# Performance work log

Measured on AMD Instinct MI355X. Metric: run time of the kernel, lower is better.

## Reference

```python
import math
import jax, jax.numpy as jnp
import numpy as np

NUM_BUCKETS = 32
MAX_DISTANCE = 128
N_HEADS = 16
D_KV = 64


def _relative_position_bucket(relative_position, num_buckets=NUM_BUCKETS, max_distance=MAX_DISTANCE):
    # bidirectional (encoder) version, faithful to T5Attention._relative_position_bucket
    nb = num_buckets // 2
    rel_buckets = (relative_position > 0).astype(jnp.int32) * nb
    rp = jnp.abs(relative_position)
    max_exact = nb // 2
    is_small = rp < max_exact
    # log-spaced buckets for large distances; clamp arg of log to >=1 to avoid -inf
    rp_large = max_exact + (
        jnp.log(jnp.maximum(rp, 1).astype(jnp.float32) / max_exact)
        / math.log(max_distance / max_exact)
        * (nb - max_exact)
    ).astype(jnp.int32)
    rp_large = jnp.minimum(rp_large, nb - 1)
    return rel_buckets + jnp.where(is_small, rp, rp_large)


def setup_inputs() -> dict:
    key = jax.random.key(0)
    ks = jax.random.split(key, 6)
    B, S, D = 2, 2048, 1024
    scale = 0.02
    return {
        "hidden_states": jax.random.normal(ks[0], (B, S, D), dtype=jnp.float32),
        "Wq": jax.random.normal(ks[1], (D, N_HEADS * D_KV), dtype=jnp.float32) * scale,
        "Wk": jax.random.normal(ks[2], (D, N_HEADS * D_KV), dtype=jnp.float32) * scale,
        "Wv": jax.random.normal(ks[3], (D, N_HEADS * D_KV), dtype=jnp.float32) * scale,
        "Wo": jax.random.normal(ks[4], (N_HEADS * D_KV, D), dtype=jnp.float32) * scale,
        "rel_bias": jax.random.normal(ks[5], (NUM_BUCKETS, N_HEADS), dtype=jnp.float32),
    }


def reference(hidden_states, Wq, Wk, Wv, Wo, rel_bias):
    B, S, D = hidden_states.shape
    H, dk = N_HEADS, D_KV
    q = (hidden_states @ Wq).reshape(B, S, H, dk)
    k = (hidden_states @ Wk).reshape(B, S, H, dk)
    v = (hidden_states @ Wv).reshape(B, S, H, dk)

    pos = jnp.arange(S)
    relative_position = pos[None, :] - pos[:, None]          # [S_q, S_k]
    buckets = _relative_position_bucket(relative_position)    # [S_q, S_k]
    bias = rel_bias[buckets].transpose(2, 0, 1)               # [H, S_q, S_k]

    # T5 attention: NO 1/sqrt(d) scaling
    scores = jnp.einsum('bqhd,bkhd->bhqk', q, k) + bias[None]
    attn = jax.nn.softmax(scores, axis=-1)
    ctx = jnp.einsum('bhqk,bkhd->bqhd', attn, v).reshape(B, S, H * dk)
    return ctx @ Wo
```

## Files before the change

kernel.cpp:

```cpp
#include <hip/hip_runtime.h>
#include <hip/hip_bf16.h>
#include <stdint.h>

#define S_LEN 2048
#define NH 16
#define NB_DELTA (2*S_LEN-1)
#define LOG2E 1.4426950408889634f

typedef __attribute__((ext_vector_type(8))) __bf16 bf16x8;
typedef __attribute__((ext_vector_type(4))) float f32x4;

__device__ __forceinline__ unsigned short f2bf(float f){
    union { float f; unsigned int u; } v; v.f = f;
    unsigned int u = v.u;
    return (unsigned short)((u + 0x7FFFu + ((u >> 16) & 1u)) >> 16);
}
__device__ __forceinline__ float bf2f(unsigned short u){
    union { unsigned int u; float f; } v; v.u = ((unsigned int)u) << 16;
    return v.f;
}
__device__ __forceinline__ unsigned int pkbf(float a, float b){
    __hip_bfloat162 h = __float22bfloat162_rn(float2{a, b});
    unsigned int u;
    __builtin_memcpy(&u, &h, 4);
    return u;
}
#if __has_builtin(__builtin_amdgcn_exp2f)
__device__ __forceinline__ float fexp2(float x){ return __builtin_amdgcn_exp2f(x); }
#else
__device__ __forceinline__ float fexp2(float x){ return __expf(x * 0.69314718056f); }
#endif

__device__ __forceinline__ void gload16(const void* g, void* l){
    __builtin_amdgcn_global_load_lds(
        (const __attribute__((address_space(1))) void*)(uintptr_t)g,
        (__attribute__((address_space(3))) void*)(uintptr_t)l, 16, 0, 0);
}

__global__ __launch_bounds__(256) void prep_kernel(
    const float* __restrict__ hs, unsigned short* __restrict__ hsb,
    const float* __restrict__ W0, const float* __restrict__ W1,
    const float* __restrict__ W2, const float* __restrict__ W3,
    unsigned short* __restrict__ D0, unsigned short* __restrict__ D1,
    unsigned short* __restrict__ D2, unsigned short* __restrict__ D3,
    const float* __restrict__ rel_bias, float* __restrict__ biasT){
    if (blockIdx.z == 4) {
        int bi = blockIdx.y * 32 + blockIdx.x;
        for (int it = 0; it < 4; it++) {
            int i = bi * 4096 + it * 1024 + threadIdx.x * 4;
            float4 f = *(const float4*)(hs + i);
            ushort4 o;
            o.x = f2bf(f.x); o.y = f2bf(f.y); o.z = f2bf(f.z); o.w = f2bf(f.w);
            *(ushort4*)(hsb + i) = o;
        }
        if (bi < 16) {
            int t = bi * 256 + threadIdx.x;
            if (t < NB_DELTA) {
                int delta = t - (S_LEN - 1);
                int bucket = (delta > 0) ? 16 : 0;
                int a = delta < 0 ? -delta : delta;
                int b;
                if (a < 8) b = a;
                else {
                    int bl = 33 - __builtin_clz(a * a);
                    b = bl < 15 ? bl : 15;
                }
                bucket += b;
                for (int h = 0; h < NH; h++)
                    biasT[h * NB_DELTA + t] = (rel_bias[bucket * NH + h] - 16.f) * LOG2E;
            }
        }
        return;
    }
    const float* src; unsigned short* dst;
    switch (blockIdx.z) {
        case 0: src = W0; dst = D0; break;
        case 1: src = W1; dst = D1; break;
        case 2: src = W2; dst = D2; break;
        default: src = W3; dst = D3; break;
    }
    __shared__ float tile[32][33];
    int bx = blockIdx.x, by = blockIdx.y;
    int tx = threadIdx.x & 31, ty = threadIdx.x >> 5;
    for (int i = 0; i < 4; i++)
        tile[ty + 8*i][tx] = src[(size_t)(by*32 + ty + 8*i) * 1024 + bx*32 + tx];
    __syncthreads();
    for (int i = 0; i < 4; i++)
        dst[(size_t)(bx*32 + ty + 8*i) * 1024 + by*32 + tx] = f2bf(tile[tx][ty + 8*i]);
}

template<int MODE, int BM>
__global__ __launch_bounds__(256) void gemm_bt_kernel(const unsigned short* __restrict__ A,
                                                      const unsigned short* __restrict__ BT,
                                                      float* __restrict__ C0,
                                                      unsigned short* __restrict__ C1,
                                                      unsigned short* __restrict__ Vt,
                                                      int Kdim, int ldc){
    constexpr int IT = BM / 32;
    __shared__ __align__(16) unsigned short As[BM * 64];
    __shared__ __align__(16) unsigned short Bs[128 * 64];
    const int t = threadIdx.x;
    const int wave = t >> 6, lane = t & 63;
    const int quad = lane >> 4, l16 = lane & 15;
    const int wm = (wave >> 1) * (BM / 2), wn = (wave & 1) * 64;
    const size_t row0 = (size_t)blockIdx.y * BM, col0 = (size_t)blockIdx.x * 128;

    const int srow8 = lane >> 3;
    const int gg = (lane & 7) ^ srow8;
    const unsigned short* gA = A  + (row0 + wave * 8 + srow8) * (size_t)Kdim + gg * 8;
    const unsigned short* gB = BT + (col0 + wave * 8 + srow8) * (size_t)Kdim + gg * 8;

    f32x4 acc[IT][4] = {};

    for (int kt = 0; kt < Kdim; kt += 64) {
        for (int p = 0; p < BM / 32; p++)
            gload16(gA + (size_t)(p * 32) * Kdim + kt, &As[(p * 32 + wave * 8) * 64]);
        for (int p = 0; p < 4; p++)
            gload16(gB + (size_t)(p * 32) * Kdim + kt, &Bs[(p * 32 + wave * 8) * 64]);
        __syncthreads();
        bf16x8 a[2][IT], b[2][4];
        for (int ks = 0; ks < 2; ks++) {
            for (int i = 0; i < IT; i++)
                a[ks][i] = *(const bf16x8*)(&As[(wm + i*16 + l16) * 64 + (((ks*4 + quad) ^ (l16 & 7)) * 8)]);
            for (int j = 0; j < 4; j++)
                b[ks][j] = *(const bf16x8*)(&Bs[(wn + j*16 + l16) * 64 + (((ks*4 + quad) ^ (l16 & 7)) * 8)]);
        }
        for (int ks = 0; ks < 2; ks++)
            for (int i = 0; i < IT; i++)
                for (int j = 0; j < 4; j++)
                    acc[i][j] = __builtin_amdgcn_mfma_f32_16x16x32_bf16(a[ks][i], b[ks][j], acc[i][j], 0, 0, 0);
        __syncthreads();
    }
    for (int i = 0; i < IT; i++)
        for (int j = 0; j < 4; j++) {
            size_t r0 = row0 + wm + i*16 + quad*4;
            size_t c  = col0 + wn + j*16 + l16;
            if (MODE == 0) {
                for (int r = 0; r < 4; r++)
                    C0[(r0 + r) * ldc + c] = acc[i][j][r];
            } else if (c < 2048) {
                float qs = (c < 1024) ? LOG2E : 1.0f;
                for (int r = 0; r < 4; r++)
                    C1[(r0 + r) * ldc + c] = f2bf(acc[i][j][r] * qs);
            } else {
                size_t bb = r0 >> 11, s = r0 & 2047;
                ushort4 o;
                o.x = f2bf(acc[i][j][0]); o.y = f2bf(acc[i][j][1]);
                o.z = f2bf(acc[i][j][2]); o.w = f2bf(acc[i][j][3]);
                *(ushort4*)(Vt + ((bb << 10) + (c - 2048)) * 2048 + s) = o;
            }
        }
}

__global__ __launch_bounds__(512, 4) void flash13_kernel(
    const unsigned short* __restrict__ qkv,
    const unsigned short* __restrict__ vt,
    const float* __restrict__ biasT,
    unsigned short* __restrict__ ctxpb,
    float* __restrict__ rsbuf)
{
    const int qt = blockIdx.x, h = blockIdx.y;
    const int b = blockIdx.z >> 1, ck = blockIdx.z & 1;
    const int kt0 = ck << 10;
    const int t = threadIdx.x;
    const int w = t >> 6, lane = t & 63, quad = lane >> 4, l16 = lane & 15;
    const int q0 = qt * 256;

    __shared__ __align__(16) unsigned short Ks[2][64 * 64];
    __shared__ __align__(16) unsigned short Vs[2][64 * 64];
    __shared__ float bias_b[1280];

    {
        const float* bsrc = biasT + h * NB_DELTA + (kt0 - q0 + 1792);
        for (int u = t; u < 1279; u += 512) bias_b[u] = bsrc[u];
    }
    const int srow8 = lane >> 3;
    const int gg = (lane & 7) ^ srow8;
    const int swz = (l16 & 7) * 8;
    const unsigned short* kbase = qkv + (size_t)(b * S_LEN + w * 8 + srow8) * 3072 + 1024 + h * 64 + gg * 8;
    const unsigned short* vbase = vt + (size_t)(b * 1024 + h * 64 + w * 8 + srow8) * 2048 + gg * 8;
    gload16(kbase + (size_t)kt0 * 3072, &Ks[0][(w * 8) * 64]);
    gload16(vbase + kt0,                &Vs[0][(w * 8) * 64]);

    bf16x8 qb[2][2];
    {
        const unsigned short* qbase =
            qkv + (size_t)(b * S_LEN + q0 + w * 32 + l16) * 3072 + h * 64 + quad * 8;
        for (int nt = 0; nt < 2; nt++)
            for (int ks = 0; ks < 2; ks++)
                qb[ks][nt] = *(const bf16x8*)(qbase + (size_t)nt * 16 * 3072 + ks * 32);
    }
    __syncthreads();

    bf16x8 onesA = {};
    if (l16 == 0) {
        const __bf16 one = (__bf16)1.0f;
        for (int e = 0; e < 8; e++) onesA[e] = one;
    }

    f32x4 ctx[4][2] = {};
    f32x4 rsacc[2] = {};
    const int ib0 = 255 + quad * 4 - w * 32 - l16;

    int cur = 0;
    for (int i = 0; i < 16; i++) {
        if (i < 15) {
            int ktn = kt0 + (i + 1) * 64;
            gload16(kbase + (size_t)ktn * 3072, &Ks[cur ^ 1][(w * 8) * 64]);
            gload16(vbase + ktn,                &Vs[cur ^ 1][(w * 8) * 64]);
        }
        f32x4 st[4][2];
        const int ibt = ib0 + i * 64;
        for (int nt = 0; nt < 2; nt++)
            for (int nb = 0; nb < 4; nb++) {
                const float* bp = &bias_b[ibt - nt * 16 + nb * 16];
                st[nb][nt][0] = bp[0]; st[nb][nt][1] = bp[1];
                st[nb][nt][2] = bp[2]; st[nb][nt][3] = bp[3];
            }
        __builtin_amdgcn_s_setprio(1);
        for (int ks = 0; ks < 2; ks++)
            for (int nb = 0; nb < 4; nb++) {
                bf16x8 ka = *(const bf16x8*)&Ks[cur][(nb * 16 + l16) * 64 + (((ks * 4 + quad) * 8) ^ swz)];
                st[nb][0] = __builtin_amdgcn_mfma_f32_16x16x32_bf16(ka, qb[ks][0], st[nb][0], 0, 0, 0);
                st[nb][1] = __builtin_amdgcn_mfma_f32_16x16x32_bf16(ka, qb[ks][1], st[nb][1], 0, 0, 0);
            }
        __builtin_amdgcn_s_setprio(0);
        uint2 pk[2][4];
        for (int nt = 0; nt < 2; nt++)
            for (int nb = 0; nb < 4; nb++) {
                float e0 = fexp2(st[nb][nt][0]);
                float e1 = fexp2(st[nb][nt][1]);
                float e2 = fexp2(st[nb][nt][2]);
                float e3 = fexp2(st[nb][nt][3]);
                pk[nt][nb].x = pkbf(e0, e1);
                pk[nt][nb].y = pkbf(e2, e3);
            }
        __builtin_amdgcn_s_setprio(1);
        for (int ks = 0; ks < 2; ks++) {
            bf16x8 pbf[2];
            for (int nt = 0; nt < 2; nt++) {
                uint2 x0 = pk[nt][2 * ks], x1 = pk[nt][2 * ks + 1];
                auto sA = __builtin_amdgcn_permlane32_swap(x0.x, x1.x, false, false);
                auto sB = __builtin_amdgcn_permlane16_swap(sA[0], sA[1], false, false);
                auto sC = __builtin_amdgcn_permlane32_swap(x0.y, x1.y, false, false);
                auto sD = __builtin_amdgcn_permlane16_swap(sC[0], sC[1], false, false);
                unsigned int u4[4] = {sB[0], sD[0], sB[1], sD[1]};
                __builtin_memcpy(&pbf[nt], u4, 16);
            }
            rsacc[0] = __builtin_amdgcn_mfma_f32_16x16x32_bf16(onesA, pbf[0], rsacc[0], 0, 0, 0);
            rsacc[1] = __builtin_amdgcn_mfma_f32_16x16x32_bf16(onesA, pbf[1], rsacc[1], 0, 0, 0);
            for (int nd = 0; nd < 4; nd++) {
                bf16x8 va = *(const bf16x8*)&Vs[cur][(nd * 16 + l16) * 64 + (((ks * 4 + quad) * 8) ^ swz)];
                ctx[nd][0] = __builtin_amdgcn_mfma_f32_16x16x32_bf16(va, pbf[0], ctx[nd][0], 0, 0, 0);
                ctx[nd][1] = __builtin_amdgcn_mfma_f32_16x16x32_bf16(va, pbf[1], ctx[nd][1], 0, 0, 0);
            }
        }
        __builtin_amdgcn_s_setprio(0);
        __syncthreads();
        cur ^= 1;
    }
    unsigned short* cp = ctxpb + (size_t)ck * 4096 * 1024;
    for (int nt = 0; nt < 2; nt++) {
        int row = b * S_LEN + q0 + w * 32 + nt * 16 + l16;
        if (quad == 0) rsbuf[((size_t)ck * 4096 + row) * 16 + h] = rsacc[nt][0];
        for (int nd = 0; nd < 4; nd++) {
            uint2 pk2;
            pk2.x = pkbf(ctx[nd][nt][0], ctx[nd][nt][1]);
            pk2.y = pkbf(ctx[nd][nt][2], ctx[nd][nt][3]);
            *(uint2*)&cp[(size_t)row * 1024 + h * 64 + nd * 16 + quad * 4] = pk2;
        }
    }
}

__global__ __launch_bounds__(256) void combine_kernel(const unsigned short* __restrict__ ctxpb,
                                                      const float* __restrict__ rsbuf,
                                                      unsigned short* __restrict__ ctxb){
    int e = blockIdx.x * 256 + threadIdx.x;
    int row = e >> 8;
    int c4 = (e & 255) * 4;
    int h = c4 >> 6;
    float l = rsbuf[(size_t)row * 16 + h] + rsbuf[((size_t)4096 + row) * 16 + h];
    ushort4 a  = *(const ushort4*)&ctxpb[(size_t)row * 1024 + c4];
    ushort4 b2 = *(const ushort4*)&ctxpb[(size_t)4096 * 1024 + (size_t)row * 1024 + c4];
    float inv = 1.f / l;
    uint2 o;
    o.x = pkbf((bf2f(a.x) + bf2f(b2.x)) * inv, (bf2f(a.y) + bf2f(b2.y)) * inv);
    o.y = pkbf((bf2f(a.z) + bf2f(b2.z)) * inv, (bf2f(a.w) + bf2f(b2.w)) * inv);
    *(uint2*)&ctxb[(size_t)row * 1024 + c4] = o;
}

extern "C" void kernel_launch(void* const* d_in, const int* in_sizes, int n_in,
                              void* d_out, int out_size, void* d_ws, size_t ws_size,
                              hipStream_t stream) {
    const float* hs       = (const float*)d_in[0];
    const float* Wq       = (const float*)d_in[1];
    const float* Wk       = (const float*)d_in[2];
    const float* Wv       = (const float*)d_in[3];
    const float* Wo       = (const float*)d_in[4];
    const float* rel_bias = (const float*)d_in[5];
    float* out = (float*)d_out;

    char* ws = (char*)d_ws;
    float* biasT          = (float*)ws;           ws += 262144;
    unsigned short* hsb   = (unsigned short*)ws;  ws += 8388608;
    unsigned short* WT    = (unsigned short*)ws;  ws += 6291456;
    unsigned short* WoT   = (unsigned short*)ws;  ws += 2097152;
    unsigned short* qkvb  = (unsigned short*)ws;  ws += 25165824;
    unsigned short* Vtg   = (unsigned short*)ws;  ws += 8388608;
    unsigned short* ctxb  = (unsigned short*)ws;  ws += 8388608;
    unsigned short* ctxpb = (unsigned short*)ws;  ws += 16777216;
    float* rsbuf          = (float*)ws;

    prep_kernel<<<dim3(32, 32, 5), 256, 0, stream>>>(
        hs, hsb, Wq, Wk, Wv, Wo,
        WT, WT + 1024 * 1024, WT + 2 * 1024 * 1024, WoT, rel_bias, biasT);

    gemm_bt_kernel<1, 64><<<dim3(24, 64), 256, 0, stream>>>(hsb, WT, nullptr, qkvb, Vtg, 1024, 3072);
    flash13_kernel<<<dim3(S_LEN / 256, NH, 4), 512, 0, stream>>>(qkvb, Vtg, biasT, ctxpb, rsbuf);
    combine_kernel<<<4096, 256, 0, stream>>>(ctxpb, rsbuf, ctxb);
    gemm_bt_kernel<0, 64><<<dim3(8, 64), 256, 0, stream>>>(ctxb, WoT, out, nullptr, nullptr, 1024, 1024);
}
```

Measured before the change: 190.8 us.

## Halve flash query tile to 128 rows and remap blocks across XCDs

The flash attention kernel now handles 128 query rows per block instead of 256, with each wave owning 16 rows. This halves per-thread accumulator registers, and launch bounds rise to 8 blocks per CU. The grid is flattened to 1024 blocks with an XCD-aware remap (lin&7)*128 + lin>>3, so neighbouring logical tiles that share K/V land on the same XCD. The cost is that K/V tiles are loaded from global memory twice as often per query row, and each MFMA on a K fragment is reused for one query tile instead of two.

```diff
diff --git a/kernel.cpp b/kernel.cpp
--- a/kernel.cpp
+++ b/kernel.cpp
@@ -152,27 +152,30 @@
         }
 }
 
-__global__ __launch_bounds__(512, 4) void flash13_kernel(
+__global__ __launch_bounds__(512, 8) void flash14_kernel(
     const unsigned short* __restrict__ qkv,
     const unsigned short* __restrict__ vt,
     const float* __restrict__ biasT,
     unsigned short* __restrict__ ctxpb,
     float* __restrict__ rsbuf)
 {
-    const int qt = blockIdx.x, h = blockIdx.y;
-    const int b = blockIdx.z >> 1, ck = blockIdx.z & 1;
+    const int lin  = blockIdx.x;
+    const int logi = (lin & 7) * 128 + (lin >> 3);
+    const int qt = logi & 15, h = (logi >> 4) & 15;
+    const int zz = logi >> 8;
+    const int b = zz >> 1, ck = zz & 1;
     const int kt0 = ck << 10;
     const int t = threadIdx.x;
     const int w = t >> 6, lane = t & 63, quad = lane >> 4, l16 = lane & 15;
-    const int q0 = qt * 256;
+    const int q0 = qt * 128;
 
     __shared__ __align__(16) unsigned short Ks[2][64 * 64];
     __shared__ __align__(16) unsigned short Vs[2][64 * 64];
-    __shared__ float bias_b[1280];
+    __shared__ float bias_b[1152];
 
     {
-        const float* bsrc = biasT + h * NB_DELTA + (kt0 - q0 + 1792);
-        for (int u = t; u < 1279; u += 512) bias_b[u] = bsrc[u];
+        const float* bsrc = biasT + h * NB_DELTA + (kt0 - q0 + 1920);
+        for (int u = t; u < 1152; u += 512) bias_b[u] = bsrc[u];
     }
     const int srow8 = lane >> 3;
     const int gg = (lane & 7) ^ srow8;
@@ -182,13 +185,12 @@
     gload16(kbase + (size_t)kt0 * 3072, &Ks[0][(w * 8) * 64]);
     gload16(vbase + kt0,                &Vs[0][(w * 8) * 64]);
 
-    bf16x8 qb[2][2];
+    bf16x8 qb[2];
     {
         const unsigned short* qbase =
-            qkv + (size_t)(b * S_LEN + q0 + w * 32 + l16) * 3072 + h * 64 + quad * 8;
-        for (int nt = 0; nt < 2; nt++)
-            for (int ks = 0; ks < 2; ks++)
-                qb[ks][nt] = *(const bf16x8*)(qbase + (size_t)nt * 16 * 3072 + ks * 32);
+            qkv + (size_t)(b * S_LEN + q0 + w * 16 + l16) * 3072 + h * 64 + quad * 8;
+        qb[0] = *(const bf16x8*)(qbase);
+        qb[1] = *(const bf16x8*)(qbase + 32);
     }
     __syncthreads();
 
@@ -198,9 +200,9 @@
         for (int e = 0; e < 8; e++) onesA[e] = one;
     }
 
-    f32x4 ctx[4][2] = {};
-    f32x4 rsacc[2] = {};
-    const int ib0 = 255 + quad * 4 - w * 32 - l16;
+    f32x4 ctx[4] = {};
+    f32x4 rsacc = {};
+    const int ib0 = 127 + quad * 4 - w * 16 - l16;
 
     int cur = 0;
     for (int i = 0; i < 16; i++) {
@@ -209,50 +211,43 @@
             gload16(kbase + (size_t)ktn * 3072, &Ks[cur ^ 1][(w * 8) * 64]);
             gload16(vbase + ktn,                &Vs[cur ^ 1][(w * 8) * 64]);
         }
-        f32x4 st[4][2];
+        f32x4 st[4];
         const int ibt = ib0 + i * 64;
-        for (int nt = 0; nt < 2; nt++)
-            for (int nb = 0; nb < 4; nb++) {
-                const float* bp = &bias_b[ibt - nt * 16 + nb * 16];
-                st[nb][nt][0] = bp[0]; st[nb][nt][1] = bp[1];
-                st[nb][nt][2] = bp[2]; st[nb][nt][3] = bp[3];
-            }
+        for (int nb = 0; nb < 4; nb++) {
+            const float* bp = &bias_b[ibt + nb * 16];
+            st[nb][0] = bp[0]; st[nb][1] = bp[1];
+            st[nb][2] = bp[2]; st[nb][3] = bp[3];
+        }
         __builtin_amdgcn_s_setprio(1);
         for (int ks = 0; ks < 2; ks++)
             for (int nb = 0; nb < 4; nb++) {
                 bf16x8 ka = *(const bf16x8*)&Ks[cur][(nb * 16 + l16) * 64 + (((ks * 4 + quad) * 8) ^ swz)];
-                st[nb][0] = __builtin_amdgcn_mfma_f32_16x16x32_bf16(ka, qb[ks][0], st[nb][0], 0, 0, 0);
-                st[nb][1] = __builtin_amdgcn_mfma_f32_16x16x32_bf16(ka, qb[ks][1], st[nb][1], 0, 0, 0);
+                st[nb] = __builtin_amdgcn_mfma_f32_16x16x32_bf16(ka, qb[ks], st[nb], 0, 0, 0);
             }
         __builtin_amdgcn_s_setprio(0);
-        uint2 pk[2][4];
-        for (int nt = 0; nt < 2; nt++)
-            for (int nb = 0; nb < 4; nb++) {
-                float e0 = fexp2(st[nb][nt][0]);
-                float e1 = fexp2(st[nb][nt][1]);
-                float e2 = fexp2(st[nb][nt][2]);
-                float e3 = fexp2(st[nb][nt][3]);
-                pk[nt][nb].x = pkbf(e0, e1);
-                pk[nt][nb].y = pkbf(e2, e3);
-            }
+        uint2 pk[4];
+        for (int nb = 0; nb < 4; nb++) {
+            float e0 = fexp2(st[nb][0]);
+            float e1 = fexp2(st[nb][1]);
+            float e2 = fexp2(st[nb][2]);
+            float e3 = fexp2(st[nb][3]);
+            pk[nb].x = pkbf(e0, e1);
+            pk[nb].y = pkbf(e2, e3);
+        }
         __builtin_amdgcn_s_setprio(1);
         for (int ks = 0; ks < 2; ks++) {
-            bf16x8 pbf[2];
-            for (int nt = 0; nt < 2; nt++) {
-                uint2 x0 = pk[nt][2 * ks], x1 = pk[nt][2 * ks + 1];
-                auto sA = __builtin_amdgcn_permlane32_swap(x0.x, x1.x, false, false);
-                auto sB = __builtin_amdgcn_permlane16_swap(sA[0], sA[1], false, false);
-                auto sC = __builtin_amdgcn_permlane32_swap(x0.y, x1.y, false, false);
-                auto sD = __builtin_amdgcn_permlane16_swap(sC[0], sC[1], false, false);
-                unsigned int u4[4] = {sB[0], sD[0], sB[1], sD[1]};
-                __builtin_memcpy(&pbf[nt], u4, 16);
-            }
-            rsacc[0] = __builtin_amdgcn_mfma_f32_16x16x32_bf16(onesA, pbf[0], rsacc[0], 0, 0, 0);
-            rsacc[1] = __builtin_amdgcn_mfma_f32_16x16x32_bf16(onesA, pbf[1], rsacc[1], 0, 0, 0);
+            uint2 x0 = pk[2 * ks], x1 = pk[2 * ks + 1];
+            auto sA = __builtin_amdgcn_permlane32_swap(x0.x, x1.x, false, false);
+            auto sB = __builtin_amdgcn_permlane16_swap(sA[0], sA[1], false, false);
+            auto sC = __builtin_amdgcn_permlane32_swap(x0.y, x1.y, false, false);
+            auto sD = __builtin_amdgcn_permlane16_swap(sC[0], sC[1], false, false);
+            unsigned int u4[4] = {sB[0], sD[0], sB[1], sD[1]};
+            bf16x8 pbf;
+            __builtin_memcpy(&pbf, u4, 16);
+            rsacc = __builtin_amdgcn_mfma_f32_16x16x32_bf16(onesA, pbf, rsacc, 0, 0, 0);
             for (int nd = 0; nd < 4; nd++) {
                 bf16x8 va = *(const bf16x8*)&Vs[cur][(nd * 16 + l16) * 64 + (((ks * 4 + quad) * 8) ^ swz)];
-                ctx[nd][0] = __builtin_amdgcn_mfma_f32_16x16x32_bf16(va, pbf[0], ctx[nd][0], 0, 0, 0);
-                ctx[nd][1] = __builtin_amdgcn_mfma_f32_16x16x32_bf16(va, pbf[1], ctx[nd][1], 0, 0, 0);
+                ctx[nd] = __builtin_amdgcn_mfma_f32_16x16x32_bf16(va, pbf, ctx[nd], 0, 0, 0);
             }
         }
         __builtin_amdgcn_s_setprio(0);
@@ -260,13 +255,13 @@
         cur ^= 1;
     }
     unsigned short* cp = ctxpb + (size_t)ck * 4096 * 1024;
-    for (int nt = 0; nt < 2; nt++) {
-        int row = b * S_LEN + q0 + w * 32 + nt * 16 + l16;
-        if (quad == 0) rsbuf[((size_t)ck * 4096 + row) * 16 + h] = rsacc[nt][0];
+    {
+        int row = b * S_LEN + q0 + w * 16 + l16;
+        if (quad == 0) rsbuf[((size_t)ck * 4096 + row) * 16 + h] = rsacc[0];
         for (int nd = 0; nd < 4; nd++) {
             uint2 pk2;
-            pk2.x = pkbf(ctx[nd][nt][0], ctx[nd][nt][1]);
-            pk2.y = pkbf(ctx[nd][nt][2], ctx[nd][nt][3]);
+            pk2.x = pkbf(ctx[nd][0], ctx[nd][1]);
+            pk2.y = pkbf(ctx[nd][2], ctx[nd][3]);
             *(uint2*)&cp[(size_t)row * 1024 + h * 64 + nd * 16 + quad * 4] = pk2;
         }
     }
@@ -316,7 +311,7 @@
         WT, WT + 1024 * 1024, WT + 2 * 1024 * 1024, WoT, rel_bias, biasT);
 
     gemm_bt_kernel<1, 64><<<dim3(24, 64), 256, 0, stream>>>(hsb, WT, nullptr, qkvb, Vtg, 1024, 3072);
-    flash13_kernel<<<dim3(S_LEN / 256, NH, 4), 512, 0, stream>>>(qkvb, Vtg, biasT, ctxpb, rsbuf);
+    flash14_kernel<<<dim3(1024), 512, 0, stream>>>(qkvb, Vtg, biasT, ctxpb, rsbuf);
     combine_kernel<<<4096, 256, 0, stream>>>(ctxpb, rsbuf, ctxb);
     gemm_bt_kernel<0, 64><<<dim3(8, 64), 256, 0, stream>>>(ctxb, WoT, out, nullptr, nullptr, 1024, 1024);
 }
```

After: 205.2 us. 1.08x slower.

## Split attention keys into four chunks, swizzle block order, compact QK buffer

Applied to the files above, without the earlier changes.

The flash attention kernel now splits the key range into four 512-key chunks instead of two. This doubles the block count to 1024, launched as a 1D grid whose index is remapped so neighbouring blocks land on different XCDs or heads. The QK projection buffer drops the unused V columns, so its row stride shrinks from 3072 to 2048. The combine kernel sums four partials instead of two. The finer split adds more partial-context traffic and combine work in exchange for more parallelism, and the context buffer reuses the hsb workspace.

```diff
diff --git a/kernel.cpp b/kernel.cpp
--- a/kernel.cpp
+++ b/kernel.cpp
@@ -152,43 +152,46 @@
         }
 }
 
-__global__ __launch_bounds__(512, 4) void flash13_kernel(
-    const unsigned short* __restrict__ qkv,
+__global__ __launch_bounds__(512, 4) void flash16_kernel(
+    const unsigned short* __restrict__ qkb,
     const unsigned short* __restrict__ vt,
     const float* __restrict__ biasT,
     unsigned short* __restrict__ ctxpb,
     float* __restrict__ rsbuf)
 {
-    const int qt = blockIdx.x, h = blockIdx.y;
-    const int b = blockIdx.z >> 1, ck = blockIdx.z & 1;
-    const int kt0 = ck << 10;
+    const int lin  = blockIdx.x;
+    const int logi = (lin & 7) * 128 + (lin >> 3);
+    const int qt = logi & 7, h = (logi >> 3) & 15;
+    const int zz = logi >> 7;
+    const int b = zz >> 2, ck = zz & 3;
+    const int kt0 = ck << 9;
     const int t = threadIdx.x;
     const int w = t >> 6, lane = t & 63, quad = lane >> 4, l16 = lane & 15;
     const int q0 = qt * 256;
 
     __shared__ __align__(16) unsigned short Ks[2][64 * 64];
     __shared__ __align__(16) unsigned short Vs[2][64 * 64];
-    __shared__ float bias_b[1280];
+    __shared__ float bias_b[768];
 
     {
         const float* bsrc = biasT + h * NB_DELTA + (kt0 - q0 + 1792);
-        for (int u = t; u < 1279; u += 512) bias_b[u] = bsrc[u];
+        for (int u = t; u < 767; u += 512) bias_b[u] = bsrc[u];
     }
     const int srow8 = lane >> 3;
     const int gg = (lane & 7) ^ srow8;
     const int swz = (l16 & 7) * 8;
-    const unsigned short* kbase = qkv + (size_t)(b * S_LEN + w * 8 + srow8) * 3072 + 1024 + h * 64 + gg * 8;
+    const unsigned short* kbase = qkb + (size_t)(b * S_LEN + w * 8 + srow8) * 2048 + 1024 + h * 64 + gg * 8;
     const unsigned short* vbase = vt + (size_t)(b * 1024 + h * 64 + w * 8 + srow8) * 2048 + gg * 8;
-    gload16(kbase + (size_t)kt0 * 3072, &Ks[0][(w * 8) * 64]);
+    gload16(kbase + (size_t)kt0 * 2048, &Ks[0][(w * 8) * 64]);
     gload16(vbase + kt0,                &Vs[0][(w * 8) * 64]);
 
     bf16x8 qb[2][2];
     {
         const unsigned short* qbase =
-            qkv + (size_t)(b * S_LEN + q0 + w * 32 + l16) * 3072 + h * 64 + quad * 8;
+            qkb + (size_t)(b * S_LEN + q0 + w * 32 + l16) * 2048 + h * 64 + quad * 8;
         for (int nt = 0; nt < 2; nt++)
             for (int ks = 0; ks < 2; ks++)
-                qb[ks][nt] = *(const bf16x8*)(qbase + (size_t)nt * 16 * 3072 + ks * 32);
+                qb[ks][nt] = *(const bf16x8*)(qbase + (size_t)nt * 16 * 2048 + ks * 32);
     }
     __syncthreads();
 
@@ -203,10 +206,10 @@
     const int ib0 = 255 + quad * 4 - w * 32 - l16;
 
     int cur = 0;
-    for (int i = 0; i < 16; i++) {
-        if (i < 15) {
+    for (int i = 0; i < 8; i++) {
+        if (i < 7) {
             int ktn = kt0 + (i + 1) * 64;
-            gload16(kbase + (size_t)ktn * 3072, &Ks[cur ^ 1][(w * 8) * 64]);
+            gload16(kbase + (size_t)ktn * 2048, &Ks[cur ^ 1][(w * 8) * 64]);
             gload16(vbase + ktn,                &Vs[cur ^ 1][(w * 8) * 64]);
         }
         f32x4 st[4][2];
@@ -279,13 +282,17 @@
     int row = e >> 8;
     int c4 = (e & 255) * 4;
     int h = c4 >> 6;
-    float l = rsbuf[(size_t)row * 16 + h] + rsbuf[((size_t)4096 + row) * 16 + h];
-    ushort4 a  = *(const ushort4*)&ctxpb[(size_t)row * 1024 + c4];
-    ushort4 b2 = *(const ushort4*)&ctxpb[(size_t)4096 * 1024 + (size_t)row * 1024 + c4];
+    float l = 0.f;
+    for (int p = 0; p < 4; p++) l += rsbuf[((size_t)p * 4096 + row) * 16 + h];
+    float s0 = 0.f, s1 = 0.f, s2 = 0.f, s3 = 0.f;
+    for (int p = 0; p < 4; p++) {
+        ushort4 a = *(const ushort4*)&ctxpb[(size_t)p * 4096 * 1024 + (size_t)row * 1024 + c4];
+        s0 += bf2f(a.x); s1 += bf2f(a.y); s2 += bf2f(a.z); s3 += bf2f(a.w);
+    }
     float inv = 1.f / l;
     uint2 o;
-    o.x = pkbf((bf2f(a.x) + bf2f(b2.x)) * inv, (bf2f(a.y) + bf2f(b2.y)) * inv);
-    o.y = pkbf((bf2f(a.z) + bf2f(b2.z)) * inv, (bf2f(a.w) + bf2f(b2.w)) * inv);
+    o.x = pkbf(s0 * inv, s1 * inv);
+    o.y = pkbf(s2 * inv, s3 * inv);
     *(uint2*)&ctxb[(size_t)row * 1024 + c4] = o;
 }
 
@@ -305,18 +312,18 @@
     unsigned short* hsb   = (unsigned short*)ws;  ws += 8388608;
     unsigned short* WT    = (unsigned short*)ws;  ws += 6291456;
     unsigned short* WoT   = (unsigned short*)ws;  ws += 2097152;
-    unsigned short* qkvb  = (unsigned short*)ws;  ws += 25165824;
+    unsigned short* qkb   = (unsigned short*)ws;  ws += 16777216;
     unsigned short* Vtg   = (unsigned short*)ws;  ws += 8388608;
-    unsigned short* ctxb  = (unsigned short*)ws;  ws += 8388608;
-    unsigned short* ctxpb = (unsigned short*)ws;  ws += 16777216;
+    unsigned short* ctxpb = (unsigned short*)ws;  ws += 33554432;
     float* rsbuf          = (float*)ws;
+    unsigned short* ctxb  = hsb;
 
     prep_kernel<<<dim3(32, 32, 5), 256, 0, stream>>>(
         hs, hsb, Wq, Wk, Wv, Wo,
         WT, WT + 1024 * 1024, WT + 2 * 1024 * 1024, WoT, rel_bias, biasT);
 
-    gemm_bt_kernel<1, 64><<<dim3(24, 64), 256, 0, stream>>>(hsb, WT, nullptr, qkvb, Vtg, 1024, 3072);
-    flash13_kernel<<<dim3(S_LEN / 256, NH, 4), 512, 0, stream>>>(qkvb, Vtg, biasT, ctxpb, rsbuf);
+    gemm_bt_kernel<1, 64><<<dim3(24, 64), 256, 0, stream>>>(hsb, WT, nullptr, qkb, Vtg, 1024, 2048);
+    flash16_kernel<<<dim3(1024), 512, 0, stream>>>(qkb, Vtg, biasT, ctxpb, rsbuf);
     combine_kernel<<<4096, 256, 0, stream>>>(ctxpb, rsbuf, ctxb);
     gemm_bt_kernel<0, 64><<<dim3(8, 64), 256, 0, stream>>>(ctxb, WoT, out, nullptr, nullptr, 1024, 1024);
 }
```

After: 194.5 us. About the same (+2.0%).
